# Performance work log

Hardware: AMD Instinct MI355X
Metric: run time of the kernel (lower is better)

## Reference

```python
import jax, jax.numpy as jnp
import numpy as np

D_L = 64
HIDDEN = 64
CUBE = (D_L + 1) ** 3  # 274625


def setup_inputs() -> dict:
    key = jax.random.key(0)
    ks = jax.random.split(key, 9)
    B = 512
    l = jax.random.normal(ks[0], (B, D_L), dtype=jnp.float32)
    a = jax.random.normal(ks[1], (B, D_L), dtype=jnp.float32)
    v = jax.random.normal(ks[2], (B, D_L), dtype=jnp.float32)
    # Linear params (xavier-ish scale)
    W1 = jax.random.normal(ks[3], (CUBE, HIDDEN), dtype=jnp.float32) * (1.0 / np.sqrt(CUBE))
    b1 = jnp.zeros((HIDDEN,), dtype=jnp.float32)
    W2 = jax.random.normal(ks[4], (HIDDEN, HIDDEN), dtype=jnp.float32) * (1.0 / np.sqrt(HIDDEN))
    b2 = jnp.zeros((HIDDEN,), dtype=jnp.float32)
    W3 = jax.random.normal(ks[5], (HIDDEN, D_L), dtype=jnp.float32) * (1.0 / np.sqrt(HIDDEN))
    b3 = jnp.zeros((D_L,), dtype=jnp.float32)
    return {"l": l, "a": a, "v": v, "W1": W1, "b1": b1, "W2": W2, "b2": b2, "W3": W3, "b3": b3}


def reference(l, a, v, W1, b1, W2, b2, W3, b3):
    B = a.shape[0]
    ones = jnp.ones((B, 1), dtype=a.dtype)
    a_h = jnp.concatenate([ones, a], axis=1)  # [B, d+1]
    v_h = jnp.concatenate([ones, v], axis=1)
    t_h = jnp.concatenate([ones, l], axis=1)
    # fusion[b, i, j, k] = a_h[b,i] * v_h[b,j] * t_h[b,k]; flattened row-major (i,j,k)
    fusion = jnp.einsum('bi,bj,bk->bijk', a_h, v_h, t_h).reshape(B, -1)  # [B, (d+1)^3]
    h = jnp.tanh(fusion @ W1 + b1)
    h = jnp.tanh(h @ W2 + b2)
    out = jnp.tanh(h @ W3 + b3)
    return out
```

## Files before the change

kernel.cpp:

```cpp
#include <hip/hip_runtime.h>
#include <hip/hip_fp16.h>


typedef _Float16 f16;
typedef f16 f16x8 __attribute__((ext_vector_type(8)));
typedef f16 f16x2 __attribute__((ext_vector_type(2)));
typedef float fx4 __attribute__((ext_vector_type(4)));
typedef unsigned int u32;

#define WS_AT    0
#define WS_VT    131072
#define WS_PART  262144

__device__ __forceinline__ void load_lds16(const float* g, float* lds) {
  __builtin_amdgcn_global_load_lds((const __attribute__((address_space(1))) u32*)g,
                                   (__attribute__((address_space(3))) u32*)lds, 16, 0, 0);
}

__device__ __forceinline__ void seg_decode(int s, int& ia, int& iv, int& isel,
                                           int& rowbase, int& rowstride) {
  if (s < 4096)      { int i = s >> 6, j = s & 63; ia = i; iv = j; isel = 0;
                       rowbase = (i+1)*4225 + (j+1)*65 + 1; rowstride = 1; }
  else if (s < 4160) { int i = s - 4096; ia = i; iv = -1; isel = 2;
                       rowbase = (i+1)*4225 + 65; rowstride = 65; }
  else if (s < 4224) { int i = s - 4160; ia = i; iv = -1; isel = 0;
                       rowbase = (i+1)*4225 + 1; rowstride = 1; }
  else if (s < 4288) { int j = s - 4224; ia = -1; iv = j; isel = 0;
                       rowbase = (j+1)*65 + 1; rowstride = 1; }
  else if (s == 4288){ ia = -1; iv = -1; isel = 1; rowbase = 4225; rowstride = 4225; }
  else if (s == 4289){ ia = -1; iv = -1; isel = 2; rowbase = 65;   rowstride = 65; }
  else if (s == 4290){ ia = -1; iv = -1; isel = 0; rowbase = 1;    rowstride = 1; }
  else               { ia = -2; iv = -1; isel = 0; rowbase = 1;    rowstride = 1; }
}

__device__ __forceinline__ f16x8 cvt8(fx4 x0, fx4 x1) {
  f16x8 f;
  f[0]=(f16)x0[0]; f[1]=(f16)x0[1]; f[2]=(f16)x0[2]; f[3]=(f16)x0[3];
  f[4]=(f16)x1[0]; f[5]=(f16)x1[1]; f[6]=(f16)x1[2]; f[7]=(f16)x1[3];
  return f;
}
__device__ __forceinline__ f16x8 cvt8s(float a0,float a1,float a2,float a3,
                                       float a4,float a5,float a6,float a7){
  f16x8 f; f[0]=(f16)a0; f[1]=(f16)a1; f[2]=(f16)a2; f[3]=(f16)a3;
  f[4]=(f16)a4; f[5]=(f16)a5; f[6]=(f16)a6; f[7]=(f16)a7; return f;
}

__global__ __launch_bounds__(256) void prep_kernel(
    const float* __restrict__ a, const float* __restrict__ v,
    float* __restrict__ aT, float* __restrict__ vT)
{
  int g = blockIdx.x * 256 + threadIdx.x;
  int which = g >> 15;
  int idx = g & 32767;
  if (which == 0) aT[idx] = a[((idx & 511) << 6) + (idx >> 9)];
  else            vT[idx] = v[((idx & 511) << 6) + (idx >> 9)];
}

__global__ __launch_bounds__(256, 2) void fusion_gemm(
    const float* __restrict__ W1,
    const float* __restrict__ aT, const float* __restrict__ vT,
    const float* __restrict__ a, const float* __restrict__ v, const float* __restrict__ l,
    f16* __restrict__ partials)
{
  __shared__ float sbuf[4][4096];
  __shared__ f16 pl_all[17][256];

  const int tid  = threadIdx.x;
  const int bid  = blockIdx.x;
  const int grp  = bid >> 4;
  const int rr   = bid & 15;
  const int half = rr >> 3;
  const int slot = rr & 7;
  const int chunk = (grp << 3) + slot;
  const int lane = tid & 63;
  const int wave = tid >> 6;
  const int l15  = lane & 15;
  const int l4   = lane >> 4;
  const int segbase = chunk * 17;
  const int row0 = half << 8;

  #pragma unroll
  for (int t = 0; t < 17; ++t) {
    int s = segbase + t, ia, iv, is_, rb, rs;
    seg_decode(s, ia, iv, is_, rb, rs);
    float spa = (ia >= 0) ? aT[(ia << 9) + row0 + tid] : (ia == -1 ? 1.0f : 0.0f);
    float spv = (iv >= 0) ? vT[(iv << 9) + row0 + tid] : 1.0f;
    pl_all[t][tid] = (f16)(spa * spv);
  }

  f16x8 lfrag[4][2], vfrag[4][2];
  #pragma unroll
  for (int mt = 0; mt < 4; ++mt) {
    int row = row0 + (wave << 6) + (mt << 4) + l15;
    #pragma unroll
    for (int ks = 0; ks < 2; ++ks) {
      const float* pl_ = l + (row << 6) + (ks << 5) + (l4 << 3);
      lfrag[mt][ks] = cvt8(*(const fx4*)pl_, *(const fx4*)(pl_ + 4));
      const float* pv_ = v + (row << 6) + (ks << 5) + (l4 << 3);
      vfrag[mt][ks] = cvt8(*(const fx4*)pv_, *(const fx4*)(pv_ + 4));
    }
  }

  fx4 acc[4][4] = {};

#define STAGE(T, BUF) do {                                                   \
    int s_ = segbase + (T), ia_, iv_, is_, rb_, rs_;                         \
    seg_decode(s_, ia_, iv_, is_, rb_, rs_);                                 \
    _Pragma("unroll")                                                        \
    for (int h_ = 0; h_ < 4; ++h_) {                                         \
      int c_  = (h_ << 8) + (wave << 6) + lane;                              \
      int k_  = c_ >> 4;                                                     \
      int n4_ = ((c_ & 15) - 2 * (k_ >> 3)) & 15;                            \
      const float* g_ = W1 + (size_t)(rb_ + k_ * rs_) * 64 + (n4_ << 2);     \
      load_lds16(g_, &sbuf[BUF][((h_ << 8) + (wave << 6)) << 2]);            \
    }                                                                        \
  } while (0)

  asm volatile("s_waitcnt lgkmcnt(0)\n\ts_barrier" ::: "memory");

  STAGE(0, 0); STAGE(1, 1); STAGE(2, 2);

  #pragma unroll 1
  for (int t = 0; t < 17; ++t) {
    if (t < 15)       asm volatile("s_waitcnt vmcnt(8)\n\ts_barrier" ::: "memory");
    else if (t == 15) asm volatile("s_waitcnt vmcnt(4)\n\ts_barrier" ::: "memory");
    else              asm volatile("s_waitcnt vmcnt(0)\n\ts_barrier" ::: "memory");
    __builtin_amdgcn_sched_barrier(0);

    if (t + 3 < 17) {
      switch ((t + 3) & 3) {
        case 0: STAGE(t + 3, 0); break;
        case 1: STAGE(t + 3, 1); break;
        case 2: STAGE(t + 3, 2); break;
        case 3: STAGE(t + 3, 3); break;
      }
    }

    int s = segbase + t;
    int isel = ((s >= 4096 && s < 4160) || s == 4289) ? 2 : (s == 4288 ? 1 : 0);
    const float* bufc = sbuf[t & 3];

    __builtin_amdgcn_s_setprio(1);
    #pragma unroll
    for (int ks = 0; ks < 2; ++ks) {
      f16x8 bf[4];
      #pragma unroll
      for (int nt = 0; nt < 4; ++nt) {
        int n = (nt << 4) + l15;
        int col4 = ((n >> 2) + 2 * ((ks << 2) + l4)) & 15;
        int dw = (((ks << 5) + (l4 << 3)) << 6) + (col4 << 2) + (n & 3);
        bf[nt] = cvt8s(bufc[dw],       bufc[dw + 64],  bufc[dw + 128], bufc[dw + 192],
                       bufc[dw + 256], bufc[dw + 320], bufc[dw + 384], bufc[dw + 448]);
      }
      #pragma unroll
      for (int mt = 0; mt < 4; ++mt) {
        int lrow = (wave << 6) + (mt << 4) + l15;
        f16 ps = pl_all[t][lrow];
        f16x8 lv;
        if (isel == 0)      lv = lfrag[mt][ks];
        else if (isel == 2) lv = vfrag[mt][ks];
        else { const float* p_ = a + ((row0 + lrow) << 6) + (ks << 5) + (l4 << 3);
               lv = cvt8(*(const fx4*)p_, *(const fx4*)(p_ + 4)); }
        f16x2 ps2 = { ps, ps };
        f16x8 av;
        ((f16x2*)&av)[0] = ((f16x2*)&lv)[0] * ps2;
        ((f16x2*)&av)[1] = ((f16x2*)&lv)[1] * ps2;
        ((f16x2*)&av)[2] = ((f16x2*)&lv)[2] * ps2;
        ((f16x2*)&av)[3] = ((f16x2*)&lv)[3] * ps2;
        #pragma unroll
        for (int nt = 0; nt < 4; ++nt)
          acc[mt][nt] = __builtin_amdgcn_mfma_f32_16x16x32_f16(av, bf[nt], acc[mt][nt], 0, 0, 0);
      }
    }
    __builtin_amdgcn_s_setprio(0);
  }
#undef STAGE

  __syncthreads();
  f16* eb = (f16*)&sbuf[0][0];
  #pragma unroll
  for (int mt = 0; mt < 4; ++mt)
    #pragma unroll
    for (int nt = 0; nt < 4; ++nt)
      #pragma unroll
      for (int r = 0; r < 4; ++r) {
        int lrow = (wave << 6) + (mt << 4) + (l4 << 2) + r;
        int n = (nt << 4) + l15;
        eb[(lrow << 6) + n] = (f16)acc[mt][nt][r];
      }
  __syncthreads();
  {
    f16* gbase = partials + (((size_t)((chunk << 1) + half)) << 14);
    #pragma unroll
    for (int j = 0; j < 8; ++j) {
      int c = (j << 8) + tid;
      f16x8 vv = *(const f16x8*)(eb + (c << 3));
      *(f16x8*)(gbase + (c << 3)) = vv;
    }
  }
}

__global__ __launch_bounds__(256) void tail_kernel(
    const f16* __restrict__ partials, const float* __restrict__ W1, const float* __restrict__ b1,
    const float* __restrict__ W2, const float* __restrict__ b2,
    const float* __restrict__ W3, const float* __restrict__ b3, float* __restrict__ out)
{
  __shared__ float red[4][64];
  __shared__ float hbuf[64];
  __shared__ float h2buf[64];
  const int row = blockIdx.x;
  const int t = threadIdx.x;
  const int q = t >> 6, n = t & 63;
  const int half = row >> 8, lrow = row & 255;
  const f16* base = partials + ((size_t)half << 14) + ((size_t)lrow << 6) + n;

  float s0 = 0.f, s1 = 0.f, s2 = 0.f, s3 = 0.f;
  #pragma unroll 4
  for (int c = q; c < 256; c += 16) {
    s0 += (float)base[(size_t)c << 15];
    s1 += (float)base[(size_t)(c + 4) << 15];
    s2 += (float)base[(size_t)(c + 8) << 15];
    s3 += (float)base[(size_t)(c + 12) << 15];
  }
  red[q][n] = (s0 + s1) + (s2 + s3);
  __syncthreads();
  if (t < 64) {
    float acc = b1[t] + W1[t] + red[0][t] + red[1][t] + red[2][t] + red[3][t];
    hbuf[t] = tanhf(acc);
  }
  __syncthreads();
  if (t < 64) {
    float acc = b2[t];
    #pragma unroll 8
    for (int k = 0; k < 64; ++k) acc += hbuf[k] * W2[(k << 6) + t];
    h2buf[t] = tanhf(acc);
  }
  __syncthreads();
  if (t < 64) {
    float acc = b3[t];
    #pragma unroll 8
    for (int k = 0; k < 64; ++k) acc += h2buf[k] * W3[(k << 6) + t];
    out[(row << 6) + t] = tanhf(acc);
  }
}

extern "C" void kernel_launch(void* const* d_in, const int* in_sizes, int n_in,
                              void* d_out, int out_size, void* d_ws, size_t ws_size,
                              hipStream_t stream) {
  const float* l  = (const float*)d_in[0];
  const float* a  = (const float*)d_in[1];
  const float* v  = (const float*)d_in[2];
  const float* W1 = (const float*)d_in[3];
  const float* b1 = (const float*)d_in[4];
  const float* W2 = (const float*)d_in[5];
  const float* b2 = (const float*)d_in[6];
  const float* W3 = (const float*)d_in[7];
  const float* b3 = (const float*)d_in[8];
  float* out = (float*)d_out;

  char* ws = (char*)d_ws;
  float* aT = (float*)(ws + WS_AT);
  float* vT = (float*)(ws + WS_VT);
  f16* partials = (f16*)(ws + WS_PART);

  hipLaunchKernelGGL(prep_kernel, dim3(256), dim3(256), 0, stream, a, v, aT, vT);
  hipLaunchKernelGGL(fusion_gemm, dim3(512), dim3(256), 0, stream,
                     W1, aT, vT, a, v, l, partials);
  hipLaunchKernelGGL(tail_kernel, dim3(512), dim3(256), 0, stream,
                     partials, W1, b1, W2, b2, W3, b3, out);
}
```

Measured before the change: 63.66 us.

## Stage W1 via registers as fp16 in LDS with 512-thread blocks covering all rows

Each block now processes all 512 batch rows for its 17-segment chunk with 512 threads, halving the grid so every W1 slice is read from global memory once instead of twice. W1 tiles are loaded into registers, converted to fp16 and written to padded, swizzled LDS buffers in a few large batches separated by barriers. This replaces the async global-to-LDS fp32 ring buffer and the per-element fp32 LDS reads plus conversions. The risks are fewer blocks in flight (256 on the GPU), a coarse-grained batch pipeline with poorer load/compute overlap, and higher register and LDS pressure.

```diff
diff --git a/kernel.cpp b/kernel.cpp
--- a/kernel.cpp
+++ b/kernel.cpp
@@ -6,16 +6,10 @@
 typedef f16 f16x8 __attribute__((ext_vector_type(8)));
 typedef f16 f16x2 __attribute__((ext_vector_type(2)));
 typedef float fx4 __attribute__((ext_vector_type(4)));
-typedef unsigned int u32;
 
 #define WS_AT    0
 #define WS_VT    131072
 #define WS_PART  262144
-
-__device__ __forceinline__ void load_lds16(const float* g, float* lds) {
-  __builtin_amdgcn_global_load_lds((const __attribute__((address_space(1))) u32*)g,
-                                   (__attribute__((address_space(3))) u32*)lds, 16, 0, 0);
-}
 
 __device__ __forceinline__ void seg_decode(int s, int& ia, int& iv, int& isel,
                                            int& rowbase, int& rowstride) {
@@ -39,11 +33,6 @@
   f[4]=(f16)x1[0]; f[5]=(f16)x1[1]; f[6]=(f16)x1[2]; f[7]=(f16)x1[3];
   return f;
 }
-__device__ __forceinline__ f16x8 cvt8s(float a0,float a1,float a2,float a3,
-                                       float a4,float a5,float a6,float a7){
-  f16x8 f; f[0]=(f16)a0; f[1]=(f16)a1; f[2]=(f16)a2; f[3]=(f16)a3;
-  f[4]=(f16)a4; f[5]=(f16)a5; f[6]=(f16)a6; f[7]=(f16)a7; return f;
-}
 
 __global__ __launch_bounds__(256) void prep_kernel(
     const float* __restrict__ a, const float* __restrict__ v,
@@ -56,128 +45,137 @@
   else            vT[idx] = v[((idx & 511) << 6) + (idx >> 9)];
 }
 
-__global__ __launch_bounds__(256, 2) void fusion_gemm(
+__device__ __forceinline__ void compute_seg(
+    int t, int segbase, const f16* __restrict__ buf,
+    const f16 (* __restrict__ pl_all)[512],
+    const f16x8 (&lfrag)[4][2],
+    const float* __restrict__ a, const float* __restrict__ v,
+    int wave, int l15, int l4, fx4 (&acc)[4][4])
+{
+  int s = segbase + t;
+  int isel = ((s >= 4096 && s < 4160) || s == 4289) ? 2 : (s == 4288 ? 1 : 0);
+  #pragma unroll
+  for (int ks = 0; ks < 2; ++ks) {
+    f16x8 bf[4];
+    #pragma unroll
+    for (int nt = 0; nt < 4; ++nt) {
+      int n = (nt << 4) + l15;
+      int c2 = (((ks << 2) + l4) + (n >> 3)) & 7;
+      bf[nt] = *(const f16x8*)((const char*)buf + n * 144 + (c2 << 4));
+    }
+    #pragma unroll
+    for (int mt = 0; mt < 4; ++mt) {
+      int lrow = (wave << 6) + (mt << 4) + l15;
+      f16 ps = pl_all[t][lrow];
+      f16x8 lv;
+      if (isel == 0) lv = lfrag[mt][ks];
+      else {
+        const float* p = (isel == 1 ? a : v) + ((size_t)lrow << 6) + (ks << 5) + (l4 << 3);
+        lv = cvt8(*(const fx4*)p, *(const fx4*)(p + 4));
+      }
+      f16x2 ps2 = { ps, ps };
+      f16x8 av;
+      ((f16x2*)&av)[0] = ((f16x2*)&lv)[0] * ps2;
+      ((f16x2*)&av)[1] = ((f16x2*)&lv)[1] * ps2;
+      ((f16x2*)&av)[2] = ((f16x2*)&lv)[2] * ps2;
+      ((f16x2*)&av)[3] = ((f16x2*)&lv)[3] * ps2;
+      #pragma unroll
+      for (int nt = 0; nt < 4; ++nt)
+        acc[mt][nt] = __builtin_amdgcn_mfma_f32_16x16x32_f16(av, bf[nt], acc[mt][nt], 0, 0, 0);
+    }
+  }
+}
+
+__global__ __launch_bounds__(512, 2) void fusion_gemm(
     const float* __restrict__ W1,
     const float* __restrict__ aT, const float* __restrict__ vT,
     const float* __restrict__ a, const float* __restrict__ v, const float* __restrict__ l,
     f16* __restrict__ partials)
 {
-  __shared__ float sbuf[4][4096];
-  __shared__ f16 pl_all[17][256];
+  __shared__ f16 bufs[15][4608];
+  __shared__ f16 pl_all[17][512];
 
   const int tid  = threadIdx.x;
-  const int bid  = blockIdx.x;
-  const int grp  = bid >> 4;
-  const int rr   = bid & 15;
-  const int half = rr >> 3;
-  const int slot = rr & 7;
-  const int chunk = (grp << 3) + slot;
+  const int chunk= blockIdx.x;
   const int lane = tid & 63;
   const int wave = tid >> 6;
   const int l15  = lane & 15;
   const int l4   = lane >> 4;
   const int segbase = chunk * 17;
-  const int row0 = half << 8;
+  const int kst  = tid >> 3;
+  const int ngst = tid & 7;
+
+  fx4 st[8][2];
+
+#define ISSUE(J, T) do {                                                      \
+    int s_ = segbase + (T), ia_, iv_, is_, rb_, rs_;                          \
+    seg_decode(s_, ia_, iv_, is_, rb_, rs_);                                  \
+    const float* g_ = W1 + (size_t)(rb_ + kst * rs_) * 64 + (ngst << 3);      \
+    st[J][0] = *(const fx4*)g_;                                               \
+    st[J][1] = *(const fx4*)(g_ + 4);                                         \
+  } while (0)
+
+#define WRITESEG(J, BUF) do {                                                 \
+    int c2_ = ((kst >> 3) + ngst) & 7;                                        \
+    char* base_ = (char*)&bufs[BUF][0] + (size_t)(ngst << 3) * 144            \
+                  + (c2_ << 4) + ((kst & 7) << 1);                            \
+    _Pragma("unroll")                                                         \
+    for (int e_ = 0; e_ < 8; ++e_)                                            \
+      *(f16*)(base_ + e_ * 144) = (f16)st[J][e_ >> 2][e_ & 3];                \
+  } while (0)
+
+  ISSUE(0, 0); ISSUE(1, 1); ISSUE(2, 2); ISSUE(3, 3);
+  ISSUE(4, 4); ISSUE(5, 5); ISSUE(6, 6); ISSUE(7, 7);
 
   #pragma unroll
   for (int t = 0; t < 17; ++t) {
     int s = segbase + t, ia, iv, is_, rb, rs;
     seg_decode(s, ia, iv, is_, rb, rs);
-    float spa = (ia >= 0) ? aT[(ia << 9) + row0 + tid] : (ia == -1 ? 1.0f : 0.0f);
-    float spv = (iv >= 0) ? vT[(iv << 9) + row0 + tid] : 1.0f;
+    float spa = (ia >= 0) ? aT[(ia << 9) + tid] : (ia == -1 ? 1.0f : 0.0f);
+    float spv = (iv >= 0) ? vT[(iv << 9) + tid] : 1.0f;
     pl_all[t][tid] = (f16)(spa * spv);
   }
 
-  f16x8 lfrag[4][2], vfrag[4][2];
+  f16x8 lfrag[4][2];
   #pragma unroll
   for (int mt = 0; mt < 4; ++mt) {
-    int row = row0 + (wave << 6) + (mt << 4) + l15;
+    int row = (wave << 6) + (mt << 4) + l15;
     #pragma unroll
     for (int ks = 0; ks < 2; ++ks) {
-      const float* pl_ = l + (row << 6) + (ks << 5) + (l4 << 3);
-      lfrag[mt][ks] = cvt8(*(const fx4*)pl_, *(const fx4*)(pl_ + 4));
-      const float* pv_ = v + (row << 6) + (ks << 5) + (l4 << 3);
-      vfrag[mt][ks] = cvt8(*(const fx4*)pv_, *(const fx4*)(pv_ + 4));
+      const float* p = l + ((size_t)row << 6) + (ks << 5) + (l4 << 3);
+      lfrag[mt][ks] = cvt8(*(const fx4*)p, *(const fx4*)(p + 4));
     }
   }
 
   fx4 acc[4][4] = {};
 
-#define STAGE(T, BUF) do {                                                   \
-    int s_ = segbase + (T), ia_, iv_, is_, rb_, rs_;                         \
-    seg_decode(s_, ia_, iv_, is_, rb_, rs_);                                 \
-    _Pragma("unroll")                                                        \
-    for (int h_ = 0; h_ < 4; ++h_) {                                         \
-      int c_  = (h_ << 8) + (wave << 6) + lane;                              \
-      int k_  = c_ >> 4;                                                     \
-      int n4_ = ((c_ & 15) - 2 * (k_ >> 3)) & 15;                            \
-      const float* g_ = W1 + (size_t)(rb_ + k_ * rs_) * 64 + (n4_ << 2);     \
-      load_lds16(g_, &sbuf[BUF][((h_ << 8) + (wave << 6)) << 2]);            \
-    }                                                                        \
-  } while (0)
-
-  asm volatile("s_waitcnt lgkmcnt(0)\n\ts_barrier" ::: "memory");
-
-  STAGE(0, 0); STAGE(1, 1); STAGE(2, 2);
-
+  WRITESEG(0, 0); WRITESEG(1, 1); WRITESEG(2, 2); WRITESEG(3, 3);
+  WRITESEG(4, 4); WRITESEG(5, 5); WRITESEG(6, 6); WRITESEG(7, 7);
+  __syncthreads();
+
+  ISSUE(0, 8); ISSUE(1, 9); ISSUE(2, 10); ISSUE(3, 11);
+  ISSUE(4, 12); ISSUE(5, 13); ISSUE(6, 14);
   #pragma unroll 1
-  for (int t = 0; t < 17; ++t) {
-    if (t < 15)       asm volatile("s_waitcnt vmcnt(8)\n\ts_barrier" ::: "memory");
-    else if (t == 15) asm volatile("s_waitcnt vmcnt(4)\n\ts_barrier" ::: "memory");
-    else              asm volatile("s_waitcnt vmcnt(0)\n\ts_barrier" ::: "memory");
-    __builtin_amdgcn_sched_barrier(0);
-
-    if (t + 3 < 17) {
-      switch ((t + 3) & 3) {
-        case 0: STAGE(t + 3, 0); break;
-        case 1: STAGE(t + 3, 1); break;
-        case 2: STAGE(t + 3, 2); break;
-        case 3: STAGE(t + 3, 3); break;
-      }
-    }
-
-    int s = segbase + t;
-    int isel = ((s >= 4096 && s < 4160) || s == 4289) ? 2 : (s == 4288 ? 1 : 0);
-    const float* bufc = sbuf[t & 3];
-
-    __builtin_amdgcn_s_setprio(1);
-    #pragma unroll
-    for (int ks = 0; ks < 2; ++ks) {
-      f16x8 bf[4];
-      #pragma unroll
-      for (int nt = 0; nt < 4; ++nt) {
-        int n = (nt << 4) + l15;
-        int col4 = ((n >> 2) + 2 * ((ks << 2) + l4)) & 15;
-        int dw = (((ks << 5) + (l4 << 3)) << 6) + (col4 << 2) + (n & 3);
-        bf[nt] = cvt8s(bufc[dw],       bufc[dw + 64],  bufc[dw + 128], bufc[dw + 192],
-                       bufc[dw + 256], bufc[dw + 320], bufc[dw + 384], bufc[dw + 448]);
-      }
-      #pragma unroll
-      for (int mt = 0; mt < 4; ++mt) {
-        int lrow = (wave << 6) + (mt << 4) + l15;
-        f16 ps = pl_all[t][lrow];
-        f16x8 lv;
-        if (isel == 0)      lv = lfrag[mt][ks];
-        else if (isel == 2) lv = vfrag[mt][ks];
-        else { const float* p_ = a + ((row0 + lrow) << 6) + (ks << 5) + (l4 << 3);
-               lv = cvt8(*(const fx4*)p_, *(const fx4*)(p_ + 4)); }
-        f16x2 ps2 = { ps, ps };
-        f16x8 av;
-        ((f16x2*)&av)[0] = ((f16x2*)&lv)[0] * ps2;
-        ((f16x2*)&av)[1] = ((f16x2*)&lv)[1] * ps2;
-        ((f16x2*)&av)[2] = ((f16x2*)&lv)[2] * ps2;
-        ((f16x2*)&av)[3] = ((f16x2*)&lv)[3] * ps2;
-        #pragma unroll
-        for (int nt = 0; nt < 4; ++nt)
-          acc[mt][nt] = __builtin_amdgcn_mfma_f32_16x16x32_f16(av, bf[nt], acc[mt][nt], 0, 0, 0);
-      }
-    }
-    __builtin_amdgcn_s_setprio(0);
-  }
-#undef STAGE
-
-  __syncthreads();
-  f16* eb = (f16*)&sbuf[0][0];
+  for (int t = 0; t < 8; ++t)
+    compute_seg(t, segbase, &bufs[t][0], pl_all, lfrag, a, v, wave, l15, l4, acc);
+  WRITESEG(0, 8); WRITESEG(1, 9); WRITESEG(2, 10); WRITESEG(3, 11);
+  WRITESEG(4, 12); WRITESEG(5, 13); WRITESEG(6, 14);
+  __syncthreads();
+
+  ISSUE(0, 15); ISSUE(1, 16);
+  #pragma unroll 1
+  for (int t = 8; t < 15; ++t)
+    compute_seg(t, segbase, &bufs[t][0], pl_all, lfrag, a, v, wave, l15, l4, acc);
+  WRITESEG(0, 0); WRITESEG(1, 1);
+  __syncthreads();
+
+  compute_seg(15, segbase, &bufs[0][0], pl_all, lfrag, a, v, wave, l15, l4, acc);
+  compute_seg(16, segbase, &bufs[1][0], pl_all, lfrag, a, v, wave, l15, l4, acc);
+#undef ISSUE
+#undef WRITESEG
+
+  __syncthreads();
+  f16* eb = &bufs[0][0];
   #pragma unroll
   for (int mt = 0; mt < 4; ++mt)
     #pragma unroll
@@ -190,12 +188,11 @@
       }
   __syncthreads();
   {
-    f16* gbase = partials + (((size_t)((chunk << 1) + half)) << 14);
+    f16* gbase = partials + ((size_t)chunk << 15);
     #pragma unroll
     for (int j = 0; j < 8; ++j) {
-      int c = (j << 8) + tid;
-      f16x8 vv = *(const f16x8*)(eb + (c << 3));
-      *(f16x8*)(gbase + (c << 3)) = vv;
+      int c = (j << 9) + tid;
+      *(f16x8*)(gbase + ((size_t)c << 3)) = *(const f16x8*)(eb + (c << 3));
     }
   }
 }
@@ -211,8 +208,7 @@
   const int row = blockIdx.x;
   const int t = threadIdx.x;
   const int q = t >> 6, n = t & 63;
-  const int half = row >> 8, lrow = row & 255;
-  const f16* base = partials + ((size_t)half << 14) + ((size_t)lrow << 6) + n;
+  const f16* base = partials + ((size_t)row << 6) + n;
 
   float s0 = 0.f, s1 = 0.f, s2 = 0.f, s3 = 0.f;
   #pragma unroll 4
@@ -264,7 +260,7 @@
   f16* partials = (f16*)(ws + WS_PART);
 
   hipLaunchKernelGGL(prep_kernel, dim3(256), dim3(256), 0, stream, a, v, aT, vT);
-  hipLaunchKernelGGL(fusion_gemm, dim3(512), dim3(256), 0, stream,
+  hipLaunchKernelGGL(fusion_gemm, dim3(256), dim3(512), 0, stream,
                      W1, aT, vT, a, v, l, partials);
   hipLaunchKernelGGL(tail_kernel, dim3(512), dim3(256), 0, stream,
                      partials, W1, b1, W2, b2, W3, b3, out);
```

Measured after the change: 98.42 us. 1.55x slower.
